# Kernel tuning notes

Measured on AMD Instinct MI355X. Metric: run time of the kernel, lower is better.

The kernel has to match this reference:

```python
import jax, jax.numpy as jnp
import numpy as np
from jax import lax

EPS = 0.001

def squash(t):
    # squash along last axis: ||t||^2/(1+||t||^2) * t/(eps+||t||)
    ns = jnp.sum(t * t, axis=-1, keepdims=True)
    return ns / (1.0 + ns) * (t / (EPS + jnp.sqrt(ns)))

def conv2d(x, w, b, stride):
    y = lax.conv_general_dilated(x, w, (stride, stride), 'VALID',
                                 dimension_numbers=('NCHW', 'OIHW', 'NCHW'))
    return y + b[None, :, None, None]

def setup_inputs() -> dict:
    key = jax.random.key(0)
    ks = jax.random.split(key, 12)
    B = 512
    x = jax.random.normal(ks[0], (B, 1, 28, 28), dtype=jnp.float32)
    targets = jax.random.randint(ks[1], (B,), 0, 10)
    s = lambda fan: 1.0 / np.sqrt(fan)
    Wc = jax.random.normal(ks[2], (256, 1, 9, 9), dtype=jnp.float32) * s(1 * 81)
    bc = jnp.zeros((256,), jnp.float32)
    # 32 primary-capsule convs (256->8, k9, s2) fused into one conv with 256 out channels
    Wp = jax.random.normal(ks[3], (32 * 8, 256, 9, 9), dtype=jnp.float32) * s(256 * 81)
    bp = jnp.zeros((32 * 8,), jnp.float32)
    Wd = jax.random.normal(ks[4], (1152, 10, 16, 8), dtype=jnp.float32)  # torch.randn init
    W1 = jax.random.normal(ks[5], (512, 160), dtype=jnp.float32) * s(160)
    b1 = jnp.zeros((512,), jnp.float32)
    W2 = jax.random.normal(ks[6], (1024, 512), dtype=jnp.float32) * s(512)
    b2 = jnp.zeros((1024,), jnp.float32)
    W3 = jax.random.normal(ks[7], (784, 1024), dtype=jnp.float32) * s(1024)
    b3 = jnp.zeros((784,), jnp.float32)
    return {"x": x, "targets": targets, "Wc": Wc, "bc": bc, "Wp": Wp, "bp": bp,
            "Wd": Wd, "W1": W1, "b1": b1, "W2": W2, "b2": b2, "W3": W3, "b3": b3}

def reference(x, targets, Wc, bc, Wp, bp, Wd, W1, b1, W2, b2, W3, b3):
    B = x.shape[0]
    # ConvLayer: 1->256, k9 -> [B,256,20,20]
    h = jax.nn.relu(conv2d(x, Wc, bc, 1))
    # PrimeLayerCaps: 32 parallel convs fused -> [B,256,6,6] -> [B,32,8,6,6] -> [B,1152,8]
    u = conv2d(h, Wp, bp, 2).reshape(B, 32, 8, 6, 6).reshape(B, 1152, 8)
    u = squash(u)
    # DigitLayerCaps: u_hat[b,c,j,o] = sum_i W[c,j,o,i] * u[b,c,i]  -> [B,1152,10,16]
    u_hat = jnp.einsum('cjoi,bci->bcjo', Wd, u)
    # dynamic routing, 3 iterations; agreement uses s_j (as in source)
    b_ij = jnp.zeros((B, 1152, 10), u_hat.dtype)
    iterations = 3
    for it in range(iterations):
        c_ij = jax.nn.softmax(b_ij, axis=2)                 # over 10 digit caps
        s_j = jnp.einsum('bcj,bcjo->bjo', c_ij, u_hat)      # [B,10,16]
        v_j = squash(s_j)
        if it < iterations - 1:
            b_ij = b_ij + jnp.einsum('bjo,bcjo->bcj', s_j, u_hat)
    # Decoder (training path: mask by targets)
    lengths = jnp.sqrt(jnp.sum(v_j * v_j, axis=2))          # [B,10]
    index = jnp.argmax(jax.nn.softmax(lengths, axis=1), axis=1)
    mask = jax.nn.one_hot(targets, 10, dtype=v_j.dtype)     # [B,10]
    masked = (mask[:, :, None] * v_j).reshape(B, 160)
    z = jax.nn.relu(masked @ W1.T + b1)
    z = jax.nn.relu(z @ W2.T + b2)
    recon = jax.nn.sigmoid(z @ W3.T + b3).reshape(B, 1, 28, 28)
    return v_j, recon, index
```

## Files before the change

### kernel.cpp

```cpp
#include <hip/hip_runtime.h>
#include <math.h>

typedef __attribute__((ext_vector_type(2))) double f64x2;
typedef __attribute__((ext_vector_type(4))) double f64x4;
typedef __attribute__((ext_vector_type(2))) float f32x2;
typedef __attribute__((ext_vector_type(4))) float f32x4;

__global__ __launch_bounds__(64) void k_probe(int* __restrict__ flag) {
  int l = threadIdx.x;
  int g = l >> 4, c = l & 15;
  double a = 1.0 + (double)(l & 15) + 17.0 * (double)(l >> 4);
  double b = 2.0 + 3.0 * (double)(l >> 4) + 5.0 * (double)(l & 15);
  f64x4 d = {0.0, 0.0, 0.0, 0.0};
  d = __builtin_amdgcn_mfma_f64_16x16x4f64(a, b, d, 0, 0, 0);
  auto ref = [](int R, int C) -> double {
    double s = 0.0;
    for (int k = 0; k < 4; k++) s += (1.0 + R + 17.0 * k) * (2.0 + 3.0 * k + 5.0 * C);
    return s;
  };
  int ok1 = 1, ok2 = 1, ok3 = 1, ok4 = 1;
#pragma unroll
  for (int r = 0; r < 4; r++) {
    double v = d[r];
    ok1 &= (v == ref(g * 4 + r, c));
    ok2 &= (v == ref(g + 4 * r, c));
    ok3 &= (v == ref(c, g * 4 + r));
    ok4 &= (v == ref(c, g + 4 * r));
  }
  ok1 = __all(ok1); ok2 = __all(ok2); ok3 = __all(ok3); ok4 = __all(ok4);
  if (l == 0) *flag = ok1 ? 1 : (ok2 ? 2 : (ok3 ? 3 : (ok4 ? 4 : 0)));
}

__global__ __launch_bounds__(256) void k_wkn(const float* __restrict__ Wp,
                                             float* __restrict__ wT) {
  const int total = 20736 * 256;
  for (int gid = blockIdx.x * 256 + threadIdx.x; gid < total; gid += gridDim.x * 256) {
    int k = gid >> 8, n = gid & 255;
    int t = k >> 8, ci = k & 255;
    wT[gid] = Wp[(size_t)n * 20736 + ci * 81 + t];
  }
}

__global__ __launch_bounds__(256) void k_conv1_19(const float* __restrict__ x,
                                                  const float* __restrict__ Wc,
                                                  const float* __restrict__ bc,
                                                  double* __restrict__ h) {
  int b = blockIdx.x >> 1;
  int rh = (blockIdx.x & 1) * 10;
  int re = rh ? 19 : 10;
  int oc = threadIdx.x;
  __shared__ float xs[784];
  for (int i = threadIdx.x; i < 784; i += 256) xs[i] = x[(size_t)b * 784 + i];
  __syncthreads();
  float w[81];
#pragma unroll
  for (int t = 0; t < 81; t++) w[t] = Wc[(size_t)oc * 81 + t];
  double bias = (double)bc[oc];
  for (int oh = rh; oh < re; oh++) {
    for (int ow4 = 0; ow4 < 20; ow4 += 4) {
      double a0 = bias, a1 = bias, a2 = bias, a3 = bias;
#pragma unroll
      for (int ky = 0; ky < 9; ky++) {
        const float* xr = &xs[(oh + ky) * 28 + ow4];
#pragma unroll
        for (int kx = 0; kx < 9; kx++) {
          double wv = (double)w[ky * 9 + kx];
          a0 += wv * (double)xr[kx + 0];
          a1 += wv * (double)xr[kx + 1];
          a2 += wv * (double)xr[kx + 2];
          a3 += wv * (double)xr[kx + 3];
        }
      }
      size_t base = ((size_t)(b * 19 + oh) * 19 + ow4) * 256 + oc;
      h[base + 0]   = fmax(a0, 0.0);
      h[base + 256] = fmax(a1, 0.0);
      h[base + 512] = fmax(a2, 0.0);
      if (ow4 < 16) h[base + 768] = fmax(a3, 0.0);
    }
  }
}

__global__ __launch_bounds__(256, 3) void k_conv2_m2(const double* __restrict__ h,
                                                     const float* __restrict__ wT,
                                                     double* __restrict__ uraw,
                                                     const int* __restrict__ flagp,
                                                     int mG0, int imgLo) {
  __shared__ __align__(16) double As[2][16][66];
  __shared__ __align__(16) double Bs[2][16][34];
  int tid = threadIdx.x;
  int m0 = blockIdx.x * 64, n0 = blockIdx.y * 32;

  int ma = tid & 63, kqa = tid >> 6;
  int mGa = mG0 + m0 + ma;
  int imga = mGa / 36, spa = mGa % 36;
  size_t abase = ((size_t)((imga - imgLo) * 361 + (spa / 6) * 38 + (spa % 6) * 2)) * 256;
  const double* hrow = h + abase;
  int kb = tid >> 4, np2 = (tid & 15) * 2;
  int w = tid >> 6, lane = tid & 63;
  int fl = lane & 15, fk = lane >> 4;
  int flag = *flagp;

  f64x2 pa0, pa1;
  f32x2 pb;
  auto loadreg = [&](int ks) {
    int t = ks >> 4, ci0 = (ks & 15) * 16;
    const double* ga = hrow + (size_t)((t / 9) * 19 + (t % 9)) * 256 + ci0 + kqa * 4;
    pa0 = *(const f64x2*)ga;
    pa1 = *(const f64x2*)(ga + 2);
    pb = *(const f32x2*)(wT + (size_t)(ks * 16 + kb) * 256 + n0 + np2);
  };
  auto writebuf = [&](int buf) {
    As[buf][kqa * 4 + 0][ma] = pa0.x;
    As[buf][kqa * 4 + 1][ma] = pa0.y;
    As[buf][kqa * 4 + 2][ma] = pa1.x;
    As[buf][kqa * 4 + 3][ma] = pa1.y;
    Bs[buf][kb][np2 + 0] = (double)pb.x;
    Bs[buf][kb][np2 + 1] = (double)pb.y;
  };

  loadreg(0);
  writebuf(0);
  loadreg(1);
  __syncthreads();

  if (flag) {
    f64x4 acc0 = {0, 0, 0, 0}, acc1 = {0, 0, 0, 0};
    int mwl = w * 16 + fl;
    int cur = 0;
    for (int ks = 0; ks < 1296; ks++) {
      if (ks + 1 < 1296) writebuf(cur ^ 1);
      if (ks + 2 < 1296) loadreg(ks + 2);
#pragma unroll
      for (int kq = 0; kq < 4; kq++) {
        int row = kq * 4 + fk;
        double a = As[cur][row][mwl];
        double b0 = Bs[cur][row][fl];
        double b1 = Bs[cur][row][16 + fl];
        acc0 = __builtin_amdgcn_mfma_f64_16x16x4f64(a, b0, acc0, 0, 0, 0);
        acc1 = __builtin_amdgcn_mfma_f64_16x16x4f64(a, b1, acc1, 0, 0, 0);
      }
      __syncthreads();
      cur ^= 1;
    }
    f64x4 accs[2] = {acc0, acc1};
#pragma unroll
    for (int nt = 0; nt < 2; nt++) {
#pragma unroll
      for (int r = 0; r < 4; r++) {
        int rb = (flag == 1 || flag == 3) ? (fk * 4 + r) : (fk + 4 * r);
        int R = (flag <= 2) ? rb : fl;
        int C = (flag <= 2) ? fl : rb;
        int mG = mG0 + m0 + w * 16 + R;
        int img = mG / 36, sp = mG % 36;
        int n = n0 + nt * 16 + C;
        uraw[(size_t)img * 9216 + (size_t)n * 36 + sp] = accs[nt][r];
      }
    }
  } else {
    int ty = tid >> 3, tx = tid & 7;
    double acc[2][4];
#pragma unroll
    for (int i = 0; i < 2; i++)
#pragma unroll
      for (int j = 0; j < 4; j++) acc[i][j] = 0.0;
    int cur = 0;
    for (int ks = 0; ks < 1296; ks++) {
      if (ks + 1 < 1296) writebuf(cur ^ 1);
      if (ks + 2 < 1296) loadreg(ks + 2);
#pragma unroll
      for (int kk = 0; kk < 16; kk++) {
        f64x2 av = *(const f64x2*)&As[cur][kk][ty * 2];
        f64x2 b01 = *(const f64x2*)&Bs[cur][kk][tx * 4];
        f64x2 b23 = *(const f64x2*)&Bs[cur][kk][tx * 4 + 2];
        acc[0][0] = fma(av.x, b01.x, acc[0][0]);
        acc[0][1] = fma(av.x, b01.y, acc[0][1]);
        acc[0][2] = fma(av.x, b23.x, acc[0][2]);
        acc[0][3] = fma(av.x, b23.y, acc[0][3]);
        acc[1][0] = fma(av.y, b01.x, acc[1][0]);
        acc[1][1] = fma(av.y, b01.y, acc[1][1]);
        acc[1][2] = fma(av.y, b23.x, acc[1][2]);
        acc[1][3] = fma(av.y, b23.y, acc[1][3]);
      }
      __syncthreads();
      cur ^= 1;
    }
#pragma unroll
    for (int i = 0; i < 2; i++) {
      int mG = mG0 + m0 + ty * 2 + i;
      int img = mG / 36, sp = mG % 36;
#pragma unroll
      for (int j = 0; j < 4; j++) {
        int n = n0 + tx * 4 + j;
        uraw[(size_t)img * 9216 + (size_t)n * 36 + sp] = acc[i][j];
      }
    }
  }
}

__global__ __launch_bounds__(256) void k_squash_ip(double* __restrict__ u,
                                                   const float* __restrict__ bp) {
  int idx = blockIdx.x * 256 + threadIdx.x;
  int bl = idx / 1152, c = idx % 1152;
  size_t base = ((size_t)bl * 1152 + c) * 8;
  double v[8];
  double ns = 0.0;
#pragma unroll
  for (int i = 0; i < 8; i++) {
    int f = c * 8 + i;
    int ch = f / 36;
    double val = u[base + i] + (double)bp[ch];
    v[i] = val;
    ns += val * val;
  }
  double sc = (ns / (1.0 + ns)) / (0.001 + sqrt(ns));
#pragma unroll
  for (int i = 0; i < 8; i++) u[base + i] = v[i] * sc;
}

__global__ __launch_bounds__(320) void k_uhat64(const double* __restrict__ u,
                                                const float* __restrict__ Wd,
                                                double* __restrict__ uhat, int b0) {
  int c = blockIdx.x;
  int t = threadIdx.x;
  int jo = t % 160, half = t / 160;
  double w[8];
#pragma unroll
  for (int i = 0; i < 8; i++) w[i] = (double)Wd[((size_t)c * 160 + jo) * 8 + i];
  for (int it = 0; it < 32; it++) {
    int bl = it * 2 + half;
    const double* up = u + ((size_t)(b0 + bl) * 1152 + c) * 8;
    double s = 0.0;
#pragma unroll
    for (int i = 0; i < 8; i++) s += w[i] * up[i];
    uhat[((size_t)bl * 1152 + c) * 160 + jo] = s;
  }
}

__global__ __launch_bounds__(192) void k_cij(const double* __restrict__ bij,
                                             double* __restrict__ cij) {
  int bl = blockIdx.x;
  int c = blockIdx.y * 192 + threadIdx.x;
  const double* bp_ = bij + ((size_t)bl * 1152 + c) * 10;
  double bv[10], mx = -1e300;
#pragma unroll
  for (int j = 0; j < 10; j++) { bv[j] = bp_[j]; mx = fmax(mx, bv[j]); }
  double s = 0.0;
#pragma unroll
  for (int j = 0; j < 10; j++) { bv[j] = exp(bv[j] - mx); s += bv[j]; }
  double inv = 1.0 / s;
  double* cp = cij + ((size_t)bl * 1152 + c) * 10;
#pragma unroll
  for (int j = 0; j < 10; j++) cp[j] = bv[j] * inv;
}

template <int IT>
__global__ __launch_bounds__(256) void k_route_s(const double* __restrict__ uhat,
                                                 const double* __restrict__ cij,
                                                 double* __restrict__ sj) {
  int bl = blockIdx.x, j = blockIdx.y;
  int tid = threadIdx.x;
  int o = tid & 15, cl = tid >> 4;
  double acc = 0.0;
  const double* up = uhat + (size_t)bl * 1152 * 160 + j * 16 + o;
  if (IT == 0) {
    for (int c = cl; c < 1152; c += 16) acc += 0.1 * up[(size_t)c * 160];
  } else {
    const double* cp = cij + (size_t)bl * 1152 * 10 + j;
    for (int c = cl; c < 1152; c += 16) acc += cp[(size_t)c * 10] * up[(size_t)c * 160];
  }
  __shared__ double red[256];
  red[tid] = acc;
  __syncthreads();
#pragma unroll
  for (int s = 128; s >= 16; s >>= 1) {
    if (tid < s) red[tid] += red[tid + s];
    __syncthreads();
  }
  if (tid < 16) sj[(size_t)bl * 160 + j * 16 + tid] = red[tid];
}

template <bool FIRST>
__global__ __launch_bounds__(256) void k_route_b(const double* __restrict__ uhat,
                                                 const double* __restrict__ sj,
                                                 double* __restrict__ bij) {
  __shared__ double sl[160];
  int bl = blockIdx.x;
  int tid = threadIdx.x;
  if (tid < 160) sl[tid] = sj[(size_t)bl * 160 + tid];
  __syncthreads();
  int c = blockIdx.y * 128 + (tid >> 1);
  int j0 = (tid & 1) * 5;
  const double* up = uhat + ((size_t)bl * 1152 + c) * 160;
  double* bp_ = bij + ((size_t)bl * 1152 + c) * 10;
#pragma unroll
  for (int jj = 0; jj < 5; jj++) {
    int j = j0 + jj;
    double dot = 0.0;
#pragma unroll
    for (int oo = 0; oo < 16; oo++) dot += sl[j * 16 + oo] * up[j * 16 + oo];
    bp_[j] = (FIRST ? 0.0 : bp_[j]) + dot;
  }
}

__global__ __launch_bounds__(192) void k_epi(const double* __restrict__ sj,
                                             float* __restrict__ vout,
                                             float* __restrict__ idxout, int b0) {
#pragma clang fp contract(off)
  __shared__ float vsh[160];
  __shared__ float len32[10];
  int bl = blockIdx.x;
  int tid = threadIdx.x;
  const double* sp = sj + (size_t)bl * 160;
  if (tid < 10) {
    float s32[16], a[16];
#pragma unroll
    for (int o = 0; o < 16; o++) { s32[o] = (float)sp[tid * 16 + o]; a[o] = s32[o] * s32[o]; }
    float r[8];
#pragma unroll
    for (int k = 0; k < 8; k++) r[k] = a[k] + a[k + 8];
    float ns = ((r[0] + r[1]) + (r[2] + r[3])) + ((r[4] + r[5]) + (r[6] + r[7]));
    float A = ns / (1.0f + ns);
    float D = 0.001f + sqrtf(ns);
#pragma unroll
    for (int o = 0; o < 16; o++) {
      float v = A * (s32[o] / D);
      vsh[tid * 16 + o] = v;
      a[o] = v * v;
    }
#pragma unroll
    for (int k = 0; k < 8; k++) r[k] = a[k] + a[k + 8];
    float nv = ((r[0] + r[1]) + (r[2] + r[3])) + ((r[4] + r[5]) + (r[6] + r[7]));
    len32[tid] = sqrtf(nv);
  }
  __syncthreads();
  if (tid < 160) vout[(size_t)(b0 + bl) * 160 + tid] = vsh[tid];
  if (tid == 0) {
    float mx = len32[0];
    for (int jj = 1; jj < 10; jj++) mx = fmaxf(mx, len32[jj]);
    float e[10];
    for (int jj = 0; jj < 10; jj++) e[jj] = (float)exp((double)(len32[jj] - mx));
    float ssum = ((e[0] + e[1]) + (e[2] + e[3])) + ((e[4] + e[5]) + (e[6] + e[7]));
    ssum = ssum + e[8];
    ssum = ssum + e[9];
    int best = 0;
    float bst = e[0] / ssum;
    for (int jj = 1; jj < 10; jj++) {
      float p = e[jj] / ssum;
      if (p > bst) { bst = p; best = jj; }
    }
    idxout[b0 + bl] = (float)best;
  }
}

__global__ __launch_bounds__(256) void k_z1(const float* __restrict__ vout,
                                            const int* __restrict__ targets,
                                            const float* __restrict__ W1,
                                            const float* __restrict__ b1,
                                            float* __restrict__ z1) {
  int id = blockIdx.x * 256 + threadIdx.x;
  int b = id >> 9, n = id & 511;
  int t = targets[b];
  float acc = b1[n];
  const float* wr = W1 + (size_t)n * 160 + t * 16;
  const float* vr = vout + (size_t)b * 160 + t * 16;
#pragma unroll
  for (int o = 0; o < 16; o++) acc += wr[o] * vr[o];
  z1[id] = fmaxf(acc, 0.f);
}

template <int ACT>
__global__ __launch_bounds__(256) void k_gemm_act(const float* __restrict__ Z,
                                                  const float* __restrict__ W,
                                                  const float* __restrict__ bias,
                                                  float* __restrict__ out, int N, int K) {
  __shared__ float Zt[64][17];
  __shared__ float Wt[64][17];
  int b0 = blockIdx.x * 64;
  int n0 = blockIdx.y * 64;
  int tid = threadIdx.x;
  int ty = tid >> 4, tx = tid & 15;
  int lr = tid >> 2, lc = (tid & 3) * 4;
  float acc[4][4] = {};
  for (int k0 = 0; k0 < K; k0 += 16) {
    __syncthreads();
    f32x4 zv = *(const f32x4*)(Z + (size_t)(b0 + lr) * K + k0 + lc);
    f32x4 wv = {0.f, 0.f, 0.f, 0.f};
    if (n0 + lr < N) wv = *(const f32x4*)(W + (size_t)(n0 + lr) * K + k0 + lc);
    Zt[lr][lc + 0] = zv.x; Zt[lr][lc + 1] = zv.y; Zt[lr][lc + 2] = zv.z; Zt[lr][lc + 3] = zv.w;
    Wt[lr][lc + 0] = wv.x; Wt[lr][lc + 1] = wv.y; Wt[lr][lc + 2] = wv.z; Wt[lr][lc + 3] = wv.w;
    __syncthreads();
#pragma unroll
    for (int kk = 0; kk < 16; kk++) {
      float av[4], bw[4];
#pragma unroll
      for (int i = 0; i < 4; i++) av[i] = Zt[ty * 4 + i][kk];
#pragma unroll
      for (int i = 0; i < 4; i++) bw[i] = Wt[tx * 4 + i][kk];
#pragma unroll
      for (int i = 0; i < 4; i++)
#pragma unroll
        for (int jj = 0; jj < 4; jj++) acc[i][jj] += av[i] * bw[jj];
    }
  }
#pragma unroll
  for (int i = 0; i < 4; i++)
#pragma unroll
    for (int jj = 0; jj < 4; jj++) {
      int bb = b0 + ty * 4 + i;
      int n = n0 + tx * 4 + jj;
      if (n < N) {
        float v = acc[i][jj] + bias[n];
        out[(size_t)bb * N + n] = (ACT == 0) ? fmaxf(v, 0.f) : 1.f / (1.f + __expf(-v));
      }
    }
}

extern "C" void kernel_launch(void* const* d_in, const int* in_sizes, int n_in,
                              void* d_out, int out_size, void* d_ws, size_t ws_size,
                              hipStream_t stream) {
  const float* x       = (const float*)d_in[0];
  const int* targets   = (const int*)d_in[1];
  const float* Wc      = (const float*)d_in[2];
  const float* bc      = (const float*)d_in[3];
  const float* Wp      = (const float*)d_in[4];
  const float* bp      = (const float*)d_in[5];
  const float* Wd      = (const float*)d_in[6];
  const float* W1      = (const float*)d_in[7];
  const float* b1      = (const float*)d_in[8];
  const float* W2      = (const float*)d_in[9];
  const float* b2      = (const float*)d_in[10];
  const float* W3      = (const float*)d_in[11];
  const float* b3      = (const float*)d_in[12];

  char* ws = (char*)d_ws;
  const size_t MB = 1024 * 1024;
  float* wT32 = (float*)ws;
  double* h64 = (double*)(ws + 21 * MB);
  double* u64 = (double*)(ws + 149 * MB);
  int* flagp  = (int*)(ws + 208 * MB);
  double* uhat64 = (double*)(ws);
  double* bij64  = (double*)(ws + 90 * MB);
  double* cij64  = (double*)(ws + 96 * MB);
  double* sj64   = (double*)(ws + 102 * MB);
  float* z1      = (float*)(ws + 103 * MB);
  float* z2      = (float*)(ws + 104 * MB);

  float* vout   = (float*)d_out;
  float* recon  = (float*)d_out + 81920;
  float* idxout = (float*)d_out + 81920 + 401408;

  k_probe<<<1, 64, 0, stream>>>(flagp);
  k_wkn<<<4096, 256, 0, stream>>>(Wp, wT32);
  const int iLo[3] = {0, 170, 341};
  const int iHi[3] = {171, 342, 512};
  for (int L = 0; L < 3; L++) {
    int cnt = iHi[L] - iLo[L];
    k_conv1_19<<<cnt * 2, 256, 0, stream>>>(x + (size_t)iLo[L] * 784, Wc, bc, h64);
    k_conv2_m2<<<dim3(96, 8), 256, 0, stream>>>(h64, wT32, u64, flagp, 6144 * L, iLo[L]);
  }
  k_squash_ip<<<2304, 256, 0, stream>>>(u64, bp);
  for (int e = 0; e < 8; e++) {
    int b0 = e * 64;
    k_uhat64<<<1152, 320, 0, stream>>>(u64, Wd, uhat64, b0);
    k_route_s<0><<<dim3(64, 10), 256, 0, stream>>>(uhat64, cij64, sj64);
    k_route_b<true><<<dim3(64, 9), 256, 0, stream>>>(uhat64, sj64, bij64);
    k_cij<<<dim3(64, 6), 192, 0, stream>>>(bij64, cij64);
    k_route_s<1><<<dim3(64, 10), 256, 0, stream>>>(uhat64, cij64, sj64);
    k_route_b<false><<<dim3(64, 9), 256, 0, stream>>>(uhat64, sj64, bij64);
    k_cij<<<dim3(64, 6), 192, 0, stream>>>(bij64, cij64);
    k_route_s<2><<<dim3(64, 10), 256, 0, stream>>>(uhat64, cij64, sj64);
    k_epi<<<64, 192, 0, stream>>>(sj64, vout, idxout, b0);
  }
  k_z1<<<1024, 256, 0, stream>>>(vout, targets, W1, b1, z1);
  k_gemm_act<0><<<dim3(8, 16), 256, 0, stream>>>(z1, W2, b2, z2, 1024, 512);
  k_gemm_act<1><<<dim3(8, 13), 256, 0, stream>>>(z2, W3, b3, recon, 784, 1024);
}
```

Measured before the change: 5.629 ms.

## Double conv2 K-tile depth and fuse routing softmax into agreement kernel

The primary-capsule conv GEMM now stages 32 K-rows per shared-memory tile instead of 16. This halves the number of barrier-separated iterations and widens the global loads. Separately, the c_ij softmax is fused into the b_ij update kernel, using a lane-pair shuffle for max and sum, which removes 16 kernel launches and a reread of b_ij. The larger tiles double shared-memory use per block, which may reduce occupancy at the requested 3 blocks per CU.

```diff
diff --git a/kernel.cpp b/kernel.cpp
--- a/kernel.cpp
+++ b/kernel.cpp
@@ -80,42 +80,47 @@
   }
 }
 
-__global__ __launch_bounds__(256, 3) void k_conv2_m2(const double* __restrict__ h,
+__global__ __launch_bounds__(256, 3) void k_conv2_m3(const double* __restrict__ h,
                                                      const float* __restrict__ wT,
                                                      double* __restrict__ uraw,
                                                      const int* __restrict__ flagp,
                                                      int mG0, int imgLo) {
-  __shared__ __align__(16) double As[2][16][66];
-  __shared__ __align__(16) double Bs[2][16][34];
+  __shared__ __align__(16) double As[2][32][66];
+  __shared__ __align__(16) double Bs[2][32][34];
   int tid = threadIdx.x;
   int m0 = blockIdx.x * 64, n0 = blockIdx.y * 32;
 
-  int ma = tid & 63, kqa = tid >> 6;
+  int ma = tid & 63, ko = (tid >> 6) * 8;
   int mGa = mG0 + m0 + ma;
   int imga = mGa / 36, spa = mGa % 36;
   size_t abase = ((size_t)((imga - imgLo) * 361 + (spa / 6) * 38 + (spa % 6) * 2)) * 256;
   const double* hrow = h + abase;
-  int kb = tid >> 4, np2 = (tid & 15) * 2;
+  int kb = tid >> 3, n4 = (tid & 7) * 4;
   int w = tid >> 6, lane = tid & 63;
   int fl = lane & 15, fk = lane >> 4;
   int flag = *flagp;
 
-  f64x2 pa0, pa1;
-  f32x2 pb;
+  f64x2 pa[4];
+  f32x4 pb;
   auto loadreg = [&](int ks) {
-    int t = ks >> 4, ci0 = (ks & 15) * 16;
-    const double* ga = hrow + (size_t)((t / 9) * 19 + (t % 9)) * 256 + ci0 + kqa * 4;
-    pa0 = *(const f64x2*)ga;
-    pa1 = *(const f64x2*)(ga + 2);
-    pb = *(const f32x2*)(wT + (size_t)(ks * 16 + kb) * 256 + n0 + np2);
+    int t = ks >> 3, ci0 = (ks & 7) * 32;
+    const double* ga = hrow + (size_t)((t / 9) * 19 + (t % 9)) * 256 + ci0 + ko;
+    pa[0] = *(const f64x2*)ga;
+    pa[1] = *(const f64x2*)(ga + 2);
+    pa[2] = *(const f64x2*)(ga + 4);
+    pa[3] = *(const f64x2*)(ga + 6);
+    pb = *(const f32x4*)(wT + (size_t)(ks * 32 + kb) * 256 + n0 + n4);
   };
   auto writebuf = [&](int buf) {
-    As[buf][kqa * 4 + 0][ma] = pa0.x;
-    As[buf][kqa * 4 + 1][ma] = pa0.y;
-    As[buf][kqa * 4 + 2][ma] = pa1.x;
-    As[buf][kqa * 4 + 3][ma] = pa1.y;
-    Bs[buf][kb][np2 + 0] = (double)pb.x;
-    Bs[buf][kb][np2 + 1] = (double)pb.y;
+#pragma unroll
+    for (int j = 0; j < 4; j++) {
+      As[buf][ko + 2 * j + 0][ma] = pa[j].x;
+      As[buf][ko + 2 * j + 1][ma] = pa[j].y;
+    }
+    Bs[buf][kb][n4 + 0] = (double)pb.x;
+    Bs[buf][kb][n4 + 1] = (double)pb.y;
+    Bs[buf][kb][n4 + 2] = (double)pb.z;
+    Bs[buf][kb][n4 + 3] = (double)pb.w;
   };
 
   loadreg(0);
@@ -127,11 +132,11 @@
     f64x4 acc0 = {0, 0, 0, 0}, acc1 = {0, 0, 0, 0};
     int mwl = w * 16 + fl;
     int cur = 0;
-    for (int ks = 0; ks < 1296; ks++) {
-      if (ks + 1 < 1296) writebuf(cur ^ 1);
-      if (ks + 2 < 1296) loadreg(ks + 2);
-#pragma unroll
-      for (int kq = 0; kq < 4; kq++) {
+    for (int ks = 0; ks < 648; ks++) {
+      if (ks + 1 < 648) writebuf(cur ^ 1);
+      if (ks + 2 < 648) loadreg(ks + 2);
+#pragma unroll
+      for (int kq = 0; kq < 8; kq++) {
         int row = kq * 4 + fk;
         double a = As[cur][row][mwl];
         double b0 = Bs[cur][row][fl];
@@ -164,11 +169,11 @@
 #pragma unroll
       for (int j = 0; j < 4; j++) acc[i][j] = 0.0;
     int cur = 0;
-    for (int ks = 0; ks < 1296; ks++) {
-      if (ks + 1 < 1296) writebuf(cur ^ 1);
-      if (ks + 2 < 1296) loadreg(ks + 2);
-#pragma unroll
-      for (int kk = 0; kk < 16; kk++) {
+    for (int ks = 0; ks < 648; ks++) {
+      if (ks + 1 < 648) writebuf(cur ^ 1);
+      if (ks + 2 < 648) loadreg(ks + 2);
+#pragma unroll
+      for (int kk = 0; kk < 32; kk++) {
         f64x2 av = *(const f64x2*)&As[cur][kk][ty * 2];
         f64x2 b01 = *(const f64x2*)&Bs[cur][kk][tx * 4];
         f64x2 b23 = *(const f64x2*)&Bs[cur][kk][tx * 4 + 2];
@@ -234,23 +239,6 @@
     for (int i = 0; i < 8; i++) s += w[i] * up[i];
     uhat[((size_t)bl * 1152 + c) * 160 + jo] = s;
   }
-}
-
-__global__ __launch_bounds__(192) void k_cij(const double* __restrict__ bij,
-                                             double* __restrict__ cij) {
-  int bl = blockIdx.x;
-  int c = blockIdx.y * 192 + threadIdx.x;
-  const double* bp_ = bij + ((size_t)bl * 1152 + c) * 10;
-  double bv[10], mx = -1e300;
-#pragma unroll
-  for (int j = 0; j < 10; j++) { bv[j] = bp_[j]; mx = fmax(mx, bv[j]); }
-  double s = 0.0;
-#pragma unroll
-  for (int j = 0; j < 10; j++) { bv[j] = exp(bv[j] - mx); s += bv[j]; }
-  double inv = 1.0 / s;
-  double* cp = cij + ((size_t)bl * 1152 + c) * 10;
-#pragma unroll
-  for (int j = 0; j < 10; j++) cp[j] = bv[j] * inv;
 }
 
 template <int IT>
@@ -280,9 +268,10 @@
 }
 
 template <bool FIRST>
-__global__ __launch_bounds__(256) void k_route_b(const double* __restrict__ uhat,
-                                                 const double* __restrict__ sj,
-                                                 double* __restrict__ bij) {
+__global__ __launch_bounds__(256) void k_route_bc(const double* __restrict__ uhat,
+                                                  const double* __restrict__ sj,
+                                                  double* __restrict__ bij,
+                                                  double* __restrict__ cij) {
   __shared__ double sl[160];
   int bl = blockIdx.x;
   int tid = threadIdx.x;
@@ -292,14 +281,28 @@
   int j0 = (tid & 1) * 5;
   const double* up = uhat + ((size_t)bl * 1152 + c) * 160;
   double* bp_ = bij + ((size_t)bl * 1152 + c) * 10;
+  double bv[5];
 #pragma unroll
   for (int jj = 0; jj < 5; jj++) {
     int j = j0 + jj;
     double dot = 0.0;
 #pragma unroll
     for (int oo = 0; oo < 16; oo++) dot += sl[j * 16 + oo] * up[j * 16 + oo];
-    bp_[j] = (FIRST ? 0.0 : bp_[j]) + dot;
-  }
+    bv[jj] = (FIRST ? 0.0 : bp_[j]) + dot;
+    bp_[j] = bv[jj];
+  }
+  double mx = bv[0];
+#pragma unroll
+  for (int jj = 1; jj < 5; jj++) mx = fmax(mx, bv[jj]);
+  mx = fmax(mx, __shfl_xor(mx, 1));
+  double s = 0.0;
+#pragma unroll
+  for (int jj = 0; jj < 5; jj++) { bv[jj] = exp(bv[jj] - mx); s += bv[jj]; }
+  s += __shfl_xor(s, 1);
+  double inv = 1.0 / s;
+  double* cp = cij + ((size_t)bl * 1152 + c) * 10;
+#pragma unroll
+  for (int jj = 0; jj < 5; jj++) cp[j0 + jj] = bv[jj] * inv;
 }
 
 __global__ __launch_bounds__(192) void k_epi(const double* __restrict__ sj,
@@ -456,18 +459,16 @@
   for (int L = 0; L < 3; L++) {
     int cnt = iHi[L] - iLo[L];
     k_conv1_19<<<cnt * 2, 256, 0, stream>>>(x + (size_t)iLo[L] * 784, Wc, bc, h64);
-    k_conv2_m2<<<dim3(96, 8), 256, 0, stream>>>(h64, wT32, u64, flagp, 6144 * L, iLo[L]);
+    k_conv2_m3<<<dim3(96, 8), 256, 0, stream>>>(h64, wT32, u64, flagp, 6144 * L, iLo[L]);
   }
   k_squash_ip<<<2304, 256, 0, stream>>>(u64, bp);
   for (int e = 0; e < 8; e++) {
     int b0 = e * 64;
     k_uhat64<<<1152, 320, 0, stream>>>(u64, Wd, uhat64, b0);
     k_route_s<0><<<dim3(64, 10), 256, 0, stream>>>(uhat64, cij64, sj64);
-    k_route_b<true><<<dim3(64, 9), 256, 0, stream>>>(uhat64, sj64, bij64);
-    k_cij<<<dim3(64, 6), 192, 0, stream>>>(bij64, cij64);
+    k_route_bc<true><<<dim3(64, 9), 256, 0, stream>>>(uhat64, sj64, bij64, cij64);
     k_route_s<1><<<dim3(64, 10), 256, 0, stream>>>(uhat64, cij64, sj64);
-    k_route_b<false><<<dim3(64, 9), 256, 0, stream>>>(uhat64, sj64, bij64);
-    k_cij<<<dim3(64, 6), 192, 0, stream>>>(bij64, cij64);
+    k_route_bc<false><<<dim3(64, 9), 256, 0, stream>>>(uhat64, sj64, bij64, cij64);
     k_route_s<2><<<dim3(64, 10), 256, 0, stream>>>(uhat64, cij64, sj64);
     k_epi<<<64, 192, 0, stream>>>(sj64, vout, idxout, b0);
   }
```

Measured after the change: 5.394 ms. 1.04x faster.
